# Kernel tuning notes

Measured on AMD Instinct MI355X. Metric: run time of the kernel, lower is better.

Reference implementation:

```python
import jax, jax.numpy as jnp
import numpy as np

NEG_SLOPE = 0.2
F_OUT = 64


def setup_inputs() -> dict:
    key = jax.random.key(0)
    k1, k2, k3 = jax.random.split(key, 3)
    N, F_IN = 8192, 256
    h = jax.random.normal(k1, (N, F_IN), dtype=jnp.float32)
    adj = jnp.ones((N, N), dtype=jnp.bool_)  # unused by the original forward
    # xavier-uniform-ish init scale
    W = jax.random.uniform(k2, (F_IN, F_OUT), dtype=jnp.float32,
                           minval=-1.0, maxval=1.0) * np.sqrt(6.0 / (F_IN + F_OUT))
    a = jax.random.uniform(k3, (2 * F_OUT, 1), dtype=jnp.float32,
                           minval=-1.0, maxval=1.0) * np.sqrt(6.0 / (2 * F_OUT + 1))
    return {"h": h, "adj": adj, "W": W, "a": a}


def reference(h, adj, W, a):
    # Wh: [N, F_OUT]
    Wh = h @ W
    # The torch code materializes an [N*N, F] repeat to compute what is just
    # a broadcast add of two projected score vectors:
    # e[i, j] = leakyrelu(Wh[i] @ a1 + Wh[j] @ a2)
    s1 = Wh @ a[:F_OUT]   # [N, 1]
    s2 = Wh @ a[F_OUT:]   # [N, 1]
    e = s1 + s2.T         # [N, N]
    e = jnp.where(e >= 0, e, NEG_SLOPE * e)  # LeakyReLU(0.2)
    attention = jax.nn.softmax(e, axis=1)    # note: adj is NOT used (matches source)
    return attention @ Wh                    # [N, F_OUT]
```

## Files before the change

kernel.cpp:

```cpp
#include <hip/hip_runtime.h>
#include <math.h>

#define GN 8192
#define GF 64
#define GFIN 256
#define NEG 0.2f
#define NCH 1024
#define CHSZ 8

#define OFF_WH   0
#define OFF_S1   (GN*GF)
#define OFF_S2   (OFF_S1 + GN)
#define OFF_ZS   (OFF_S2 + GN)
#define OFF_IDX  (OFF_ZS + GN)
#define OFF_VA   (OFF_IDX + GN)
#define OFF_VB   (OFF_VA + (GN+1)*GF)
#define OFF_SA   (OFF_VB + (GN+1)*GF)
#define OFF_PB   (OFF_SA + (GN+1))
#define OFF_CHA  (OFF_PB + (GN+1))
#define OFF_CHB  (OFF_CHA + NCH*GF)
#define OFF_SCA  (OFF_CHB + NCH*GF)
#define OFF_SCB  (OFF_SCA + NCH)
#define OFF_OA   (OFF_SCB + NCH)
#define OFF_OB   (OFF_OA + NCH*GF)
#define OFF_OSA  (OFF_OB + NCH*GF)
#define OFF_OSB  (OFF_OSA + NCH)

__global__ __launch_bounds__(512) void k_wh(const float* __restrict__ h,
        const float* __restrict__ W, const float* __restrict__ a,
        float* __restrict__ Wh, float* __restrict__ s1, float* __restrict__ s2) {
    __shared__ float hs[32][GFIN];
    int t = threadIdx.x;
    int row0 = blockIdx.x * 32;
    const float4* h4 = (const float4*)(h + (size_t)row0 * GFIN);
    float4* hs4 = (float4*)&hs[0][0];
    for (int i = t; i < 32*GFIN/4; i += 512) hs4[i] = h4[i];
    __syncthreads();
    int wave = t >> 6, lane = t & 63;
    float acc[4] = {0.f, 0.f, 0.f, 0.f};
    #pragma unroll 8
    for (int k = 0; k < GFIN; ++k) {
        float wv = W[k*GF + lane];
        #pragma unroll
        for (int q = 0; q < 4; ++q) acc[q] += hs[wave*4+q][k] * wv;
    }
    float a1 = a[lane], a2 = a[GF + lane];
    #pragma unroll
    for (int q = 0; q < 4; ++q) {
        int row = row0 + wave*4 + q;
        Wh[(size_t)row*GF + lane] = acc[q];
        float v1 = acc[q]*a1, v2 = acc[q]*a2;
        #pragma unroll
        for (int o = 32; o > 0; o >>= 1) { v1 += __shfl_xor(v1, o); v2 += __shfl_xor(v2, o); }
        if (lane == 0) { s1[row] = v1; s2[row] = v2; }
    }
}

__global__ __launch_bounds__(256) void k_rank(const float* __restrict__ s2v,
        float* __restrict__ zs, int* __restrict__ idx) {
    __shared__ float z[GN];
    int t = threadIdx.x;
    for (int m = t; m < GN; m += 256) z[m] = s2v[m];
    __syncthreads();
    int jl = t >> 3, s = t & 7;
    int j = blockIdx.x * 32 + jl;
    float zj = z[j];
    int cnt = 0;
    for (int i = 0; i < GN/8; ++i) {
        int m = i*8 + s;
        float zm = z[m];
        cnt += (zm < zj) || (zm == zj && m < j);
    }
    cnt += __shfl_xor(cnt, 1);
    cnt += __shfl_xor(cnt, 2);
    cnt += __shfl_xor(cnt, 4);
    if (s == 0) { zs[cnt] = zj; idx[cnt] = j; }
}

__global__ __launch_bounds__(256) void k_chunk(const float* __restrict__ Wh,
        const float* __restrict__ zs, const int* __restrict__ idx,
        float* __restrict__ chA, float* __restrict__ chB,
        float* __restrict__ scA, float* __restrict__ scB) {
    int t = threadIdx.x;
    int wave = t >> 6, lane = t & 63;
    int ch = blockIdx.x*4 + wave;
    float Z = zs[GN-1];
    float aAcc = 0.f, bAcc = 0.f, sa = 0.f, sb = 0.f;
    #pragma unroll
    for (int q = 0; q < CHSZ; ++q) {
        int r = ch*CHSZ + q;
        float zr = zs[r];
        int ir = idx[r];
        float tA = expf(zr - Z);
        float tB = expf(NEG * (zr - Z));
        float w = Wh[(size_t)ir*GF + lane];
        aAcc += tA * w; bAcc += tB * w; sa += tA; sb += tB;
    }
    chA[ch*GF + lane] = aAcc;
    chB[ch*GF + lane] = bAcc;
    if (lane == 0) { scA[ch] = sa; scB[ch] = sb; }
}

__global__ __launch_bounds__(1024) void k_scan(const float* __restrict__ chA,
        const float* __restrict__ chB, const float* __restrict__ scA,
        const float* __restrict__ scB,
        float* __restrict__ offA, float* __restrict__ offB,
        float* __restrict__ osA, float* __restrict__ osB,
        float* __restrict__ VA, float* __restrict__ VB,
        float* __restrict__ SA, float* __restrict__ PB) {
    __shared__ float buf[NCH];
    int c = blockIdx.x;
    int t = threadIdx.x;
    float vB = (c < 64) ? chB[t*GF + c] : scB[t];
    buf[t] = vB; __syncthreads();
    for (int o = 1; o < NCH; o <<= 1) {
        float y = (t >= o) ? buf[t-o] : 0.f;
        __syncthreads();
        buf[t] += y;
        __syncthreads();
    }
    float exB = (t > 0) ? buf[t-1] : 0.f;
    float totB = buf[NCH-1];
    if (c < 64) offB[t*GF + c] = exB; else osB[t] = exB;
    if (t == 0) {
        if (c < 64) { VB[(size_t)GN*GF + c] = totB; VA[(size_t)GN*GF + c] = 0.f; }
        else        { PB[GN] = totB; SA[GN] = 0.f; }
    }
    __syncthreads();
    int rt = NCH-1-t;
    float vA = (c < 64) ? chA[rt*GF + c] : scA[rt];
    buf[t] = vA; __syncthreads();
    for (int o = 1; o < NCH; o <<= 1) {
        float y = (t >= o) ? buf[t-o] : 0.f;
        __syncthreads();
        buf[t] += y;
        __syncthreads();
    }
    float exA = (t > 0) ? buf[t-1] : 0.f;
    if (c < 64) offA[rt*GF + c] = exA; else osA[rt] = exA;
}

__global__ __launch_bounds__(256) void k_fill(const float* __restrict__ Wh,
        const float* __restrict__ zs, const int* __restrict__ idx,
        const float* __restrict__ offA, const float* __restrict__ offB,
        const float* __restrict__ osA, const float* __restrict__ osB,
        float* __restrict__ VA, float* __restrict__ VB,
        float* __restrict__ SA, float* __restrict__ PB) {
    int t = threadIdx.x;
    int wave = t >> 6, lane = t & 63;
    int ch = blockIdx.x*4 + wave;
    float Z = zs[GN-1];
    float accA = offA[ch*GF + lane];
    float sAcc = osA[ch];
    #pragma unroll
    for (int q = CHSZ-1; q >= 0; --q) {
        int r = ch*CHSZ + q;
        float zr = zs[r]; int ir = idx[r];
        float w = Wh[(size_t)ir*GF + lane];
        float tA = expf(zr - Z);
        accA += tA * w; sAcc += tA;
        VA[(size_t)r*GF + lane] = accA;
        if (lane == 0) SA[r] = sAcc;
    }
    float accB = offB[ch*GF + lane];
    float sBcc = osB[ch];
    #pragma unroll
    for (int q = 0; q < CHSZ; ++q) {
        int r = ch*CHSZ + q;
        float zr = zs[r]; int ir = idx[r];
        float w = Wh[(size_t)ir*GF + lane];
        VB[(size_t)r*GF + lane] = accB;
        if (lane == 0) PB[r] = sBcc;
        float tB = expf(NEG * (zr - Z));
        accB += tB * w; sBcc += tB;
    }
}

__global__ __launch_bounds__(256) void k_out(const float* __restrict__ s1,
        const float* __restrict__ zs,
        const float* __restrict__ VA, const float* __restrict__ VB,
        const float* __restrict__ SA, const float* __restrict__ PB,
        float* __restrict__ out) {
    int t = threadIdx.x;
    int wave = t >> 6, lane = t & 63;
    int i = blockIdx.x*4 + wave;
    float s1i = s1[i];
    float Z = zs[GN-1];
    float g = s1i + Z;
    float m = (g >= 0.f) ? g : NEG*g;
    float aA = expf(g - m);
    float aB = expf(NEG*g - m);
    float tgt = -s1i;
    int lo = 0, hi = GN;
    while (lo < hi) { int mid = (lo+hi) >> 1; if (zs[mid] < tgt) lo = mid+1; else hi = mid; }
    int k = lo;
    float va = VA[(size_t)k*GF + lane];
    float vb = VB[(size_t)k*GF + lane];
    float sa = SA[k], pb = PB[k];
    out[(size_t)i*GF + lane] = (aA*va + aB*vb) / (aA*sa + aB*pb);
}

extern "C" void kernel_launch(void* const* d_in, const int* in_sizes, int n_in,
                              void* d_out, int out_size, void* d_ws, size_t ws_size,
                              hipStream_t stream) {
    const float* h = (const float*)d_in[0];
    const float* W = (const float*)d_in[2];
    const float* a = (const float*)d_in[3];
    float* ws = (float*)d_ws;
    float* Wh  = ws + OFF_WH;
    float* s1  = ws + OFF_S1;
    float* s2  = ws + OFF_S2;
    float* zs  = ws + OFF_ZS;
    int*   idx = (int*)(ws + OFF_IDX);
    float* VA  = ws + OFF_VA;
    float* VB  = ws + OFF_VB;
    float* SA  = ws + OFF_SA;
    float* PB  = ws + OFF_PB;
    float* chA = ws + OFF_CHA;
    float* chB = ws + OFF_CHB;
    float* scA = ws + OFF_SCA;
    float* scB = ws + OFF_SCB;
    float* oA  = ws + OFF_OA;
    float* oB  = ws + OFF_OB;
    float* osA = ws + OFF_OSA;
    float* osB = ws + OFF_OSB;
    float* out = (float*)d_out;

    hipLaunchKernelGGL(k_wh,    dim3(GN/32),  dim3(512),  0, stream, h, W, a, Wh, s1, s2);
    hipLaunchKernelGGL(k_rank,  dim3(GN/32),  dim3(256),  0, stream, s2, zs, idx);
    hipLaunchKernelGGL(k_chunk, dim3(NCH/4),  dim3(256),  0, stream, Wh, zs, idx, chA, chB, scA, scB);
    hipLaunchKernelGGL(k_scan,  dim3(65),     dim3(NCH),  0, stream, chA, chB, scA, scB, oA, oB, osA, osB, VA, VB, SA, PB);
    hipLaunchKernelGGL(k_fill,  dim3(NCH/4),  dim3(256),  0, stream, Wh, zs, idx, oA, oB, osA, osB, VA, VB, SA, PB);
    hipLaunchKernelGGL(k_out,   dim3(GN/4),   dim3(256),  0, stream, s1, zs, VA, VB, SA, PB, out);
}
```

Baseline: 73.15 us.

## Drop fill kernel, compute per-row prefix in output; retile projection and scan

Removes the k_fill kernel and the full-size VA/VB/SA/PB prefix arrays. k_out now finds the row's chunk by binary search, then rebuilds the partial prefix inside that chunk from the chunk offsets and Wh, so one launch and a large write/read of intermediates go away. The projection kernel now keeps W in shared memory and reads h rows straight from global memory, with 8 rows per wave. The scan uses wave shuffles with 256 threads instead of a 1024-thread barrier-heavy Hillis-Steele loop. The rank kernel uses float4 loads, and fast __expf replaces expf, which costs some accuracy. The output kernel does redundant gather work per row.

```diff
diff --git a/kernel.cpp b/kernel.cpp
--- a/kernel.cpp
+++ b/kernel.cpp
@@ -13,41 +13,40 @@
 #define OFF_S2   (OFF_S1 + GN)
 #define OFF_ZS   (OFF_S2 + GN)
 #define OFF_IDX  (OFF_ZS + GN)
-#define OFF_VA   (OFF_IDX + GN)
-#define OFF_VB   (OFF_VA + (GN+1)*GF)
-#define OFF_SA   (OFF_VB + (GN+1)*GF)
-#define OFF_PB   (OFF_SA + (GN+1))
-#define OFF_CHA  (OFF_PB + (GN+1))
+#define OFF_CHA  (OFF_IDX + GN)
 #define OFF_CHB  (OFF_CHA + NCH*GF)
 #define OFF_SCA  (OFF_CHB + NCH*GF)
 #define OFF_SCB  (OFF_SCA + NCH)
-#define OFF_OA   (OFF_SCB + NCH)
-#define OFF_OB   (OFF_OA + NCH*GF)
-#define OFF_OSA  (OFF_OB + NCH*GF)
-#define OFF_OSB  (OFF_OSA + NCH)
-
-__global__ __launch_bounds__(512) void k_wh(const float* __restrict__ h,
+#define OFF_OFA  (OFF_SCB + NCH)
+#define OFF_OFB  (OFF_OFA + (NCH+1)*GF)
+#define OFF_OSA  (OFF_OFB + (NCH+1)*GF)
+#define OFF_OSB  (OFF_OSA + (NCH+1))
+
+__global__ __launch_bounds__(256) void k_wh(const float* __restrict__ h,
         const float* __restrict__ W, const float* __restrict__ a,
         float* __restrict__ Wh, float* __restrict__ s1, float* __restrict__ s2) {
-    __shared__ float hs[32][GFIN];
-    int t = threadIdx.x;
-    int row0 = blockIdx.x * 32;
-    const float4* h4 = (const float4*)(h + (size_t)row0 * GFIN);
-    float4* hs4 = (float4*)&hs[0][0];
-    for (int i = t; i < 32*GFIN/4; i += 512) hs4[i] = h4[i];
-    __syncthreads();
-    int wave = t >> 6, lane = t & 63;
-    float acc[4] = {0.f, 0.f, 0.f, 0.f};
+    __shared__ float Wl[GFIN*GF];
+    int t = threadIdx.x;
+    int lane = t & 63;
+    const float4* W4 = (const float4*)W;
+    float4* Wl4 = (float4*)Wl;
+    #pragma unroll
+    for (int m = 0; m < 16; ++m) Wl4[t + m*256] = W4[t + m*256];
+    __syncthreads();
+    int wid = __builtin_amdgcn_readfirstlane(t >> 6);
+    int row0 = blockIdx.x * 32 + wid * 8;
+    const float* hrow = h + (size_t)row0 * GFIN;
+    float acc[8] = {0.f,0.f,0.f,0.f,0.f,0.f,0.f,0.f};
     #pragma unroll 8
     for (int k = 0; k < GFIN; ++k) {
-        float wv = W[k*GF + lane];
+        float wv = Wl[k*GF + lane];
         #pragma unroll
-        for (int q = 0; q < 4; ++q) acc[q] += hs[wave*4+q][k] * wv;
+        for (int q = 0; q < 8; ++q) acc[q] += hrow[q*GFIN + k] * wv;
     }
     float a1 = a[lane], a2 = a[GF + lane];
     #pragma unroll
-    for (int q = 0; q < 4; ++q) {
-        int row = row0 + wave*4 + q;
+    for (int q = 0; q < 8; ++q) {
+        int row = row0 + q;
         Wh[(size_t)row*GF + lane] = acc[q];
         float v1 = acc[q]*a1, v2 = acc[q]*a2;
         #pragma unroll
@@ -60,16 +59,23 @@
         float* __restrict__ zs, int* __restrict__ idx) {
     __shared__ float z[GN];
     int t = threadIdx.x;
-    for (int m = t; m < GN; m += 256) z[m] = s2v[m];
+    const float4* s4 = (const float4*)s2v;
+    float4* z4 = (float4*)z;
+    for (int m = t; m < GN/4; m += 256) z4[m] = s4[m];
     __syncthreads();
     int jl = t >> 3, s = t & 7;
     int j = blockIdx.x * 32 + jl;
     float zj = z[j];
     int cnt = 0;
-    for (int i = 0; i < GN/8; ++i) {
-        int m = i*8 + s;
-        float zm = z[m];
-        cnt += (zm < zj) || (zm == zj && m < j);
+    #pragma unroll 4
+    for (int i = 0; i < GN/32; ++i) {
+        int m4 = i*8 + s;
+        float4 v = z4[m4];
+        int mb = m4*4;
+        cnt += (v.x < zj) || (v.x == zj && mb+0 < j);
+        cnt += (v.y < zj) || (v.y == zj && mb+1 < j);
+        cnt += (v.z < zj) || (v.z == zj && mb+2 < j);
+        cnt += (v.w < zj) || (v.w == zj && mb+3 < j);
     }
     cnt += __shfl_xor(cnt, 1);
     cnt += __shfl_xor(cnt, 2);
@@ -82,8 +88,8 @@
         float* __restrict__ chA, float* __restrict__ chB,
         float* __restrict__ scA, float* __restrict__ scB) {
     int t = threadIdx.x;
-    int wave = t >> 6, lane = t & 63;
-    int ch = blockIdx.x*4 + wave;
+    int wid = t >> 6, lane = t & 63;
+    int ch = blockIdx.x*4 + wid;
     float Z = zs[GN-1];
     float aAcc = 0.f, bAcc = 0.f, sa = 0.f, sb = 0.f;
     #pragma unroll
@@ -91,112 +97,116 @@
         int r = ch*CHSZ + q;
         float zr = zs[r];
         int ir = idx[r];
-        float tA = expf(zr - Z);
-        float tB = expf(NEG * (zr - Z));
+        float d = zr - Z;
+        float tA = __expf(d);
+        float tB = __expf(NEG * d);
         float w = Wh[(size_t)ir*GF + lane];
-        aAcc += tA * w; bAcc += tB * w; sa += tA; sb += tB;
+        aAcc += tA*w; bAcc += tB*w; sa += tA; sb += tB;
     }
     chA[ch*GF + lane] = aAcc;
     chB[ch*GF + lane] = bAcc;
     if (lane == 0) { scA[ch] = sa; scB[ch] = sb; }
 }
 
-__global__ __launch_bounds__(1024) void k_scan(const float* __restrict__ chA,
+__global__ __launch_bounds__(256) void k_scan(const float* __restrict__ chA,
         const float* __restrict__ chB, const float* __restrict__ scA,
         const float* __restrict__ scB,
         float* __restrict__ offA, float* __restrict__ offB,
-        float* __restrict__ osA, float* __restrict__ osB,
-        float* __restrict__ VA, float* __restrict__ VB,
-        float* __restrict__ SA, float* __restrict__ PB) {
-    __shared__ float buf[NCH];
+        float* __restrict__ osA, float* __restrict__ osB) {
+    __shared__ float wsum[4];
+    __shared__ float wsum2[4];
     int c = blockIdx.x;
     int t = threadIdx.x;
-    float vB = (c < 64) ? chB[t*GF + c] : scB[t];
-    buf[t] = vB; __syncthreads();
-    for (int o = 1; o < NCH; o <<= 1) {
-        float y = (t >= o) ? buf[t-o] : 0.f;
-        __syncthreads();
-        buf[t] += y;
-        __syncthreads();
-    }
-    float exB = (t > 0) ? buf[t-1] : 0.f;
-    float totB = buf[NCH-1];
-    if (c < 64) offB[t*GF + c] = exB; else osB[t] = exB;
-    if (t == 0) {
-        if (c < 64) { VB[(size_t)GN*GF + c] = totB; VA[(size_t)GN*GF + c] = 0.f; }
-        else        { PB[GN] = totB; SA[GN] = 0.f; }
-    }
-    __syncthreads();
-    int rt = NCH-1-t;
-    float vA = (c < 64) ? chA[rt*GF + c] : scA[rt];
-    buf[t] = vA; __syncthreads();
-    for (int o = 1; o < NCH; o <<= 1) {
-        float y = (t >= o) ? buf[t-o] : 0.f;
-        __syncthreads();
-        buf[t] += y;
-        __syncthreads();
-    }
-    float exA = (t > 0) ? buf[t-1] : 0.f;
-    if (c < 64) offA[rt*GF + c] = exA; else osA[rt] = exA;
-}
-
-__global__ __launch_bounds__(256) void k_fill(const float* __restrict__ Wh,
+    int lane = t & 63, wid = t >> 6;
+    float v[4];
+    #pragma unroll
+    for (int q = 0; q < 4; ++q) {
+        int ch = t*4 + q;
+        v[q] = (c < 64) ? chB[ch*GF + c] : scB[ch];
+    }
+    float s = v[0]+v[1]+v[2]+v[3];
+    float ws = s;
+    #pragma unroll
+    for (int o = 1; o < 64; o <<= 1) { float y = __shfl_up(ws, o); if (lane >= o) ws += y; }
+    if (lane == 63) wsum[wid] = ws;
+    __syncthreads();
+    float blkoff = 0.f, tot = 0.f;
+    #pragma unroll
+    for (int w2 = 0; w2 < 4; ++w2) { float x = wsum[w2]; tot += x; if (w2 < wid) blkoff += x; }
+    float base = blkoff + ws - s;
+    #pragma unroll
+    for (int q = 0; q < 4; ++q) {
+        int ch = t*4 + q;
+        if (c < 64) offB[ch*GF + c] = base; else osB[ch] = base;
+        base += v[q];
+    }
+    if (t == 0) { if (c < 64) offB[NCH*GF + c] = tot; else osB[NCH] = tot; }
+    __syncthreads();
+    #pragma unroll
+    for (int q = 0; q < 4; ++q) {
+        int ch = NCH-1 - (t*4 + q);
+        v[q] = (c < 64) ? chA[ch*GF + c] : scA[ch];
+    }
+    s = v[0]+v[1]+v[2]+v[3];
+    ws = s;
+    #pragma unroll
+    for (int o = 1; o < 64; o <<= 1) { float y = __shfl_up(ws, o); if (lane >= o) ws += y; }
+    if (lane == 63) wsum2[wid] = ws;
+    __syncthreads();
+    blkoff = 0.f;
+    #pragma unroll
+    for (int w2 = 0; w2 < 4; ++w2) { float x = wsum2[w2]; if (w2 < wid) blkoff += x; }
+    base = blkoff + ws - s;
+    #pragma unroll
+    for (int q = 0; q < 4; ++q) {
+        int ch = NCH-1 - (t*4 + q);
+        if (c < 64) offA[ch*GF + c] = base; else osA[ch] = base;
+        base += v[q];
+    }
+    if (t == 0) { if (c < 64) offA[NCH*GF + c] = 0.f; else osA[NCH] = 0.f; }
+}
+
+__global__ __launch_bounds__(256) void k_out(const float* __restrict__ s1,
         const float* __restrict__ zs, const int* __restrict__ idx,
+        const float* __restrict__ Wh,
         const float* __restrict__ offA, const float* __restrict__ offB,
         const float* __restrict__ osA, const float* __restrict__ osB,
-        float* __restrict__ VA, float* __restrict__ VB,
-        float* __restrict__ SA, float* __restrict__ PB) {
-    int t = threadIdx.x;
-    int wave = t >> 6, lane = t & 63;
-    int ch = blockIdx.x*4 + wave;
-    float Z = zs[GN-1];
-    float accA = offA[ch*GF + lane];
-    float sAcc = osA[ch];
-    #pragma unroll
-    for (int q = CHSZ-1; q >= 0; --q) {
-        int r = ch*CHSZ + q;
-        float zr = zs[r]; int ir = idx[r];
-        float w = Wh[(size_t)ir*GF + lane];
-        float tA = expf(zr - Z);
-        accA += tA * w; sAcc += tA;
-        VA[(size_t)r*GF + lane] = accA;
-        if (lane == 0) SA[r] = sAcc;
-    }
-    float accB = offB[ch*GF + lane];
-    float sBcc = osB[ch];
-    #pragma unroll
-    for (int q = 0; q < CHSZ; ++q) {
-        int r = ch*CHSZ + q;
-        float zr = zs[r]; int ir = idx[r];
-        float w = Wh[(size_t)ir*GF + lane];
-        VB[(size_t)r*GF + lane] = accB;
-        if (lane == 0) PB[r] = sBcc;
-        float tB = expf(NEG * (zr - Z));
-        accB += tB * w; sBcc += tB;
-    }
-}
-
-__global__ __launch_bounds__(256) void k_out(const float* __restrict__ s1,
-        const float* __restrict__ zs,
-        const float* __restrict__ VA, const float* __restrict__ VB,
-        const float* __restrict__ SA, const float* __restrict__ PB,
         float* __restrict__ out) {
     int t = threadIdx.x;
-    int wave = t >> 6, lane = t & 63;
-    int i = blockIdx.x*4 + wave;
+    int wid = t >> 6, lane = t & 63;
+    int i = blockIdx.x*4 + wid;
     float s1i = s1[i];
     float Z = zs[GN-1];
     float g = s1i + Z;
     float m = (g >= 0.f) ? g : NEG*g;
-    float aA = expf(g - m);
-    float aB = expf(NEG*g - m);
+    float aA = __expf(g - m);
+    float aB = __expf(NEG*g - m);
     float tgt = -s1i;
     int lo = 0, hi = GN;
-    while (lo < hi) { int mid = (lo+hi) >> 1; if (zs[mid] < tgt) lo = mid+1; else hi = mid; }
+    #pragma unroll
+    for (int it = 0; it < 13; ++it) {
+        int mid = (lo + hi) >> 1;
+        if (zs[mid] < tgt) lo = mid + 1; else hi = mid;
+    }
     int k = lo;
-    float va = VA[(size_t)k*GF + lane];
-    float vb = VB[(size_t)k*GF + lane];
-    float sa = SA[k], pb = PB[k];
+    int c0 = k >> 3;
+    float va, vb, sa, pb;
+    if (c0 < NCH) {
+        va = offA[c0*GF + lane]; vb = offB[c0*GF + lane];
+        sa = osA[c0];            pb = osB[c0];
+        #pragma unroll
+        for (int q = 0; q < CHSZ; ++q) {
+            int r = c0*CHSZ + q;
+            float zr = zs[r]; int ir = idx[r];
+            float w = Wh[(size_t)ir*GF + lane];
+            float d = zr - Z;
+            if (r >= k) { float tA = __expf(d);      va += tA*w; sa += tA; }
+            else        { float tB = __expf(NEG*d);  vb += tB*w; pb += tB; }
+        }
+    } else {
+        va = 0.f; sa = 0.f;
+        vb = offB[NCH*GF + lane]; pb = osB[NCH];
+    }
     out[(size_t)i*GF + lane] = (aA*va + aB*vb) / (aA*sa + aB*pb);
 }
 
@@ -212,24 +222,19 @@
     float* s2  = ws + OFF_S2;
     float* zs  = ws + OFF_ZS;
     int*   idx = (int*)(ws + OFF_IDX);
-    float* VA  = ws + OFF_VA;
-    float* VB  = ws + OFF_VB;
-    float* SA  = ws + OFF_SA;
-    float* PB  = ws + OFF_PB;
     float* chA = ws + OFF_CHA;
     float* chB = ws + OFF_CHB;
     float* scA = ws + OFF_SCA;
     float* scB = ws + OFF_SCB;
-    float* oA  = ws + OFF_OA;
-    float* oB  = ws + OFF_OB;
+    float* ofA = ws + OFF_OFA;
+    float* ofB = ws + OFF_OFB;
     float* osA = ws + OFF_OSA;
     float* osB = ws + OFF_OSB;
     float* out = (float*)d_out;
 
-    hipLaunchKernelGGL(k_wh,    dim3(GN/32),  dim3(512),  0, stream, h, W, a, Wh, s1, s2);
-    hipLaunchKernelGGL(k_rank,  dim3(GN/32),  dim3(256),  0, stream, s2, zs, idx);
-    hipLaunchKernelGGL(k_chunk, dim3(NCH/4),  dim3(256),  0, stream, Wh, zs, idx, chA, chB, scA, scB);
-    hipLaunchKernelGGL(k_scan,  dim3(65),     dim3(NCH),  0, stream, chA, chB, scA, scB, oA, oB, osA, osB, VA, VB, SA, PB);
-    hipLaunchKernelGGL(k_fill,  dim3(NCH/4),  dim3(256),  0, stream, Wh, zs, idx, oA, oB, osA, osB, VA, VB, SA, PB);
-    hipLaunchKernelGGL(k_out,   dim3(GN/4),   dim3(256),  0, stream, s1, zs, VA, VB, SA, PB, out);
-}
+    hipLaunchKernelGGL(k_wh,    dim3(GN/32),  dim3(256), 0, stream, h, W, a, Wh, s1, s2);
+    hipLaunchKernelGGL(k_rank,  dim3(GN/32),  dim3(256), 0, stream, s2, zs, idx);
+    hipLaunchKernelGGL(k_chunk, dim3(NCH/4),  dim3(256), 0, stream, Wh, zs, idx, chA, chB, scA, scB);
+    hipLaunchKernelGGL(k_scan,  dim3(65),     dim3(256), 0, stream, chA, chB, scA, scB, ofA, ofB, osA, osB);
+    hipLaunchKernelGGL(k_out,   dim3(GN/4),   dim3(256), 0, stream, s1, zs, idx, Wh, ofA, ofB, osA, osB, out);
+}
```

Result: faster. 69.81 us (-4.6%).
